# Kernel optimization log

Measured on AMD Instinct MI355X. Metric: run time of the kernel, lower is better.

The kernel has to match this reference:

```python
import jax, jax.numpy as jnp
import numpy as np

NF = 128  # latent_dim / number of filters


def setup_inputs() -> dict:
    key = jax.random.key(0)
    k1, k2, k3, k4 = jax.random.split(key, 4)
    B, H, W, C = 4, 64, 64, 128
    x = jax.random.normal(k1, (B, H, W, C), dtype=jnp.float32)
    y = jax.random.normal(k2, (B, H, W, C), dtype=jnp.float32)
    # 1x1 conv kernels (C_in, C_out) + biases, glorot-ish scale
    scale = 1.0 / np.sqrt(C)
    W1 = jax.random.normal(k3, (C, NF), dtype=jnp.float32) * scale
    W2 = jax.random.normal(k4, (C, NF), dtype=jnp.float32) * scale
    b1 = jnp.zeros((NF,), dtype=jnp.float32)
    b2 = jnp.zeros((NF,), dtype=jnp.float32)
    return {"x": x, "y": y, "W1": W1, "b1": b1, "W2": W2, "b2": b2}


def reference(x, y, W1, b1, W2, b2):
    B, H, Wd, C = x.shape
    hw = H * Wd
    # 1x1 convs == per-pixel matmul
    xq = jnp.einsum('bhwc,cf->bhwf', x, W1) + b1   # conv1(x)
    yk = jnp.einsum('bhwc,cf->bhwf', y, W2) + b2   # conv2(y)
    xq_r = xq.reshape(B, hw, NF)
    yk_r = yk.reshape(B, hw, NF)
    # A_ij = sigmoid(y_i . x_j), full (hw x hw) sigmoid attention
    A = jax.nn.sigmoid(jnp.einsum('bic,bjc->bij', yk_r, xq_r))
    out = jnp.einsum('bij,bjc->bic', A, yk_r).reshape(B, H, Wd, NF)
    # residual add of the *projected* x (matches original: x was overwritten by conv1)
    out = out + xq
    return out
```

## Files before the change

### kernel.cpp

```cpp
#include <hip/hip_runtime.h>
#include <hip/hip_bf16.h>
#include <stdint.h>

typedef float f32x16 __attribute__((ext_vector_type(16)));
typedef float f32x4  __attribute__((ext_vector_type(4)));
typedef short s16x8  __attribute__((ext_vector_type(8)));
typedef unsigned int u32x4 __attribute__((ext_vector_type(4)));

#define HWSZ   4096
#define NBATCH 4
#define LOG2E  1.44269504088896340736f

__device__ __forceinline__ unsigned short f2bf(float f) {
    unsigned u = __builtin_bit_cast(unsigned, f);
    u += 0x7FFFu + ((u >> 16) & 1u);
    return (unsigned short)(u >> 16);
}
__device__ __forceinline__ unsigned cvt_pk_bf16(float lo, float hi) {
    __hip_bfloat162 h = __float22bfloat162_rn(make_float2(lo, hi));
    return *reinterpret_cast<unsigned*>(&h);
}
__device__ __forceinline__ float sigm2(float s) {
    return __builtin_amdgcn_rcpf(1.f + __builtin_amdgcn_exp2f(-s));
}
__device__ __forceinline__ float bf_lo(unsigned u) {
    return __builtin_bit_cast(float, u << 16);
}
__device__ __forceinline__ float bf_hi(unsigned u) {
    return __builtin_bit_cast(float, u & 0xFFFF0000u);
}
__device__ __forceinline__ float bf2f(unsigned short u) {
    return __builtin_bit_cast(float, (unsigned)u << 16);
}

template<bool WF32>
__global__ __launch_bounds__(256, 2) void proj_kernel(
    const float* __restrict__ x, const float* __restrict__ y,
    const float* __restrict__ W1, const float* __restrict__ b1,
    const float* __restrict__ W2, const float* __restrict__ b2,
    float* __restrict__ xq_f32,
    unsigned short* __restrict__ xqu_bf,
    unsigned short* __restrict__ xq_bf,
    unsigned short* __restrict__ yk_bf,
    unsigned short* __restrict__ ykT_bf)
{
    __shared__ unsigned short Xlds[32][136];
    __shared__ unsigned short Ylds[32][136];
    __shared__ unsigned short Tlds[128][40];

    const int t    = threadIdx.x;
    const int lane = t & 63;
    const int w    = t >> 6;
    const int l31  = lane & 31;
    const int g    = lane >> 5;
    const int r0   = blockIdx.x * 32;
    const int b    = r0 >> 12;
    const int j0   = r0 & (HWSZ - 1);

    #pragma unroll
    for (int i = 0; i < 4; ++i) {
        int li = t + 256 * i;
        int row = li >> 5, c = (li & 31) * 4;
        float4 vx = *(const float4*)(x + (size_t)(r0 + row) * 128 + c);
        float4 vy = *(const float4*)(y + (size_t)(r0 + row) * 128 + c);
        *(uint2*)&Xlds[row][c] = make_uint2(cvt_pk_bf16(vx.x, vx.y), cvt_pk_bf16(vx.z, vx.w));
        *(uint2*)&Ylds[row][c] = make_uint2(cvt_pk_bf16(vy.x, vy.y), cvt_pk_bf16(vy.z, vy.w));
    }
    __syncthreads();

    const int m  = w >> 1;
    const int fh = w & 1;
    const float* Wm = m ? W2 : W1;
    const float* bm = m ? b2 : b1;
    const unsigned short* A0 = m ? &Ylds[0][0] : &Xlds[0][0];

    f32x16 acc[2];
    #pragma unroll
    for (int i = 0; i < 16; ++i) { acc[0][i] = 0.f; acc[1][i] = 0.f; }

    #pragma unroll
    for (int ks = 0; ks < 8; ++ks) {
        s16x8 bfr[2];
        #pragma unroll
        for (int ft = 0; ft < 2; ++ft) {
            const float* wp = Wm + (size_t)(ks * 16 + g * 8) * 128 + fh * 64 + ft * 32 + l31;
            #pragma unroll
            for (int i = 0; i < 8; ++i)
                bfr[ft][i] = (short)f2bf(wp[(size_t)i * 128]);
        }
        s16x8 af = *(const s16x8*)(A0 + (size_t)l31 * 136 + ks * 16 + g * 8);
        acc[0] = __builtin_amdgcn_mfma_f32_32x32x16_bf16(af, bfr[0], acc[0], 0, 0, 0);
        acc[1] = __builtin_amdgcn_mfma_f32_32x32x16_bf16(af, bfr[1], acc[1], 0, 0, 0);
    }

    const float bias_v[2] = { bm[fh * 64 + l31], bm[fh * 64 + 32 + l31] };

    if (m == 0) {
        #pragma unroll
        for (int ft = 0; ft < 2; ++ft) {
            int f = fh * 64 + ft * 32 + l31;
            #pragma unroll
            for (int r = 0; r < 16; ++r) {
                int row = (r & 3) + 8 * (r >> 2) + 4 * g;
                float v = acc[ft][r] + bias_v[ft];
                size_t o = (size_t)(r0 + row) * 128 + f;
                if (WF32) xq_f32[o] = v;
                else      xqu_bf[o] = f2bf(v);
                xq_bf[o] = f2bf(v * LOG2E);
            }
        }
    } else {
        #pragma unroll
        for (int ft = 0; ft < 2; ++ft) {
            int f = fh * 64 + ft * 32 + l31;
            #pragma unroll
            for (int rg = 0; rg < 4; ++rg) {
                float p0 = acc[ft][4 * rg + 0] + bias_v[ft];
                float p1 = acc[ft][4 * rg + 1] + bias_v[ft];
                float p2 = acc[ft][4 * rg + 2] + bias_v[ft];
                float p3 = acc[ft][4 * rg + 3] + bias_v[ft];
                int jb = 8 * rg + 4 * g;
                *(uint2*)&Tlds[f][jb] = make_uint2(cvt_pk_bf16(p0, p1), cvt_pk_bf16(p2, p3));
                size_t o = (size_t)(r0 + jb) * 128 + f;
                yk_bf[o]       = f2bf(p0);
                yk_bf[o + 128] = f2bf(p1);
                yk_bf[o + 256] = f2bf(p2);
                yk_bf[o + 384] = f2bf(p3);
            }
        }
    }
    __syncthreads();

    {
        int f  = t >> 1;
        int jh = (t & 1) * 16;
        unsigned short* dst = ykT_bf + ((size_t)(b * 128 + f)) * HWSZ + j0 + jh;
        #pragma unroll
        for (int c = 0; c < 2; ++c)
            *(s16x8*)(dst + c * 8) = *(const s16x8*)&Tlds[f][jh + c * 8];
    }
}

#define KT_STR   136
#define VT_STR   72
#define KT_BYTES (64 * KT_STR * 2)
#define VT_BYTES (128 * VT_STR * 2)
#define BUF_BYTES (KT_BYTES + VT_BYTES)

__global__ __launch_bounds__(256, 2) void attn128_kernel(
    const unsigned short* __restrict__ Kbf,
    const unsigned short* __restrict__ Qbf,
    const unsigned short* __restrict__ Vtbf,
    unsigned* __restrict__ outp)
{
    __shared__ __align__(16) char smem[2 * BUF_BYTES];

    const int t    = threadIdx.x;
    const int lane = t & 63;
    const int qt   = t >> 6;
    const int l31  = lane & 31;
    const int g    = lane >> 5;

    const int split  = blockIdx.x >> 7;
    const int r      = blockIdx.x & 127;
    const int b      = r >> 5;
    const int qb     = (r & 31) * 128;
    const int jBegin = split * (HWSZ / 4);
    const int nt     = (HWSZ / 4) / 64;

    s16x8 qfrag[8];
    {
        const unsigned short* qp =
            Qbf + (((size_t)(b * HWSZ + qb + 32 * qt + l31)) << 7) + g * 8;
        #pragma unroll
        for (int fs = 0; fs < 8; ++fs)
            qfrag[fs] = *(const s16x8*)(qp + fs * 16);
    }

    f32x16 acc[4];
    #pragma unroll
    for (int ft = 0; ft < 4; ++ft)
        #pragma unroll
        for (int i = 0; i < 16; ++i) acc[ft][i] = 0.f;

    f32x16 zv;
    #pragma unroll
    for (int i = 0; i < 16; ++i) zv[i] = 0.f;

    const unsigned short* Kbase = Kbf  + (((size_t)b * HWSZ) << 7);
    const unsigned short* Vbase = Vtbf + (((size_t)b) << 7) * HWSZ;

    const unsigned short* kSrc = Kbase + (size_t)(jBegin + (t >> 4)) * 128 + (t & 15) * 8;
    const unsigned short* vSrc = Vbase + (size_t)(t >> 3) * HWSZ + jBegin + (t & 7) * 8;
    const int kDst = (t >> 4) * KT_STR + (t & 15) * 8;
    const int vDst = (t >> 3) * VT_STR + (t & 7) * 8;

    {
        unsigned short* Kl = (unsigned short*)smem;
        unsigned short* Vl = (unsigned short*)(smem + KT_BYTES);
        #pragma unroll
        for (int i = 0; i < 4; ++i)
            *(s16x8*)(Kl + kDst + i * 16 * KT_STR) = *(const s16x8*)(kSrc + (size_t)i * 2048);
        #pragma unroll
        for (int i = 0; i < 4; ++i)
            *(s16x8*)(Vl + vDst + i * 32 * VT_STR) = *(const s16x8*)(vSrc + (size_t)i * 32 * HWSZ);
    }
    __syncthreads();

    int c = 0;
    for (int it = 0; it < nt; ++it) {
        const bool pre = (it + 1 < nt);
        const unsigned short* Kl = (const unsigned short*)(smem + c * BUF_BYTES);
        const unsigned short* Vl = (const unsigned short*)(smem + c * BUF_BYTES + KT_BYTES);

        s16x8 kf0[8], kf1[8];
        {
            const unsigned short* Krow = Kl + (size_t)l31 * KT_STR + g * 8;
            #pragma unroll
            for (int fs = 0; fs < 8; ++fs)
                kf0[fs] = *(const s16x8*)(Krow + fs * 16);
        }
        f32x16 s0a, s0b;
        __builtin_amdgcn_s_setprio(1);
        #pragma unroll
        for (int fs = 0; fs < 4; ++fs) {
            s0a = __builtin_amdgcn_mfma_f32_32x32x16_bf16(kf0[fs],     qfrag[fs],
                      fs == 0 ? zv : s0a, 0, 0, 0);
            s0b = __builtin_amdgcn_mfma_f32_32x32x16_bf16(kf0[fs + 4], qfrag[fs + 4],
                      fs == 0 ? zv : s0b, 0, 0, 0);
        }
        __builtin_amdgcn_s_setprio(0);

        {
            const unsigned short* Krow = Kl + (size_t)(32 + l31) * KT_STR + g * 8;
            #pragma unroll
            for (int fs = 0; fs < 8; ++fs)
                kf1[fs] = *(const s16x8*)(Krow + fs * 16);
        }
        s16x8 kr[4], vr[4];
        if (pre) {
            kSrc += 64 * 128;
            vSrc += 64;
            #pragma unroll
            for (int i = 0; i < 4; ++i)
                kr[i] = *(const s16x8*)(kSrc + (size_t)i * 2048);
            #pragma unroll
            for (int i = 0; i < 4; ++i)
                vr[i] = *(const s16x8*)(vSrc + (size_t)i * 32 * HWSZ);
        }

        f32x16 s1a, s1b;
        unsigned W0[2][4], W1[2][4];
        #pragma unroll
        for (int fs = 0; fs < 4; ++fs) {
            s1a = __builtin_amdgcn_mfma_f32_32x32x16_bf16(kf1[fs],     qfrag[fs],
                      fs == 0 ? zv : s1a, 0, 0, 0);
            s1b = __builtin_amdgcn_mfma_f32_32x32x16_bf16(kf1[fs + 4], qfrag[fs + 4],
                      fs == 0 ? zv : s1b, 0, 0, 0);
            const int rg = fs;
            float p0 = sigm2(s0a[4 * rg + 0] + s0b[4 * rg + 0]);
            float p1 = sigm2(s0a[4 * rg + 1] + s0b[4 * rg + 1]);
            float p2 = sigm2(s0a[4 * rg + 2] + s0b[4 * rg + 2]);
            float p3 = sigm2(s0a[4 * rg + 3] + s0b[4 * rg + 3]);
            W0[0][rg] = cvt_pk_bf16(p0, p1);
            W1[0][rg] = cvt_pk_bf16(p2, p3);
        }

        __builtin_amdgcn_s_setprio(1);
        #pragma unroll
        for (int s2 = 0; s2 < 2; ++s2) {
            unsigned a0 = W0[0][2 * s2], b0 = W0[0][2 * s2 + 1];
            unsigned a1 = W1[0][2 * s2], b1 = W1[0][2 * s2 + 1];
            asm("v_permlane32_swap_b32 %0, %1" : "+v"(a0), "+v"(b0));
            asm("v_permlane32_swap_b32 %0, %1" : "+v"(a1), "+v"(b1));
            u32x4 pw;
            pw[0] = a0; pw[1] = a1; pw[2] = b0; pw[3] = b1;
            s16x8 pf = __builtin_bit_cast(s16x8, pw);
            #pragma unroll
            for (int ft = 0; ft < 4; ++ft) {
                s16x8 vf = *(const s16x8*)(Vl + (size_t)(32 * ft + l31) * VT_STR + s2 * 16 + g * 8);
                acc[ft] = __builtin_amdgcn_mfma_f32_32x32x16_bf16(pf, vf, acc[ft], 0, 0, 0);
            }
            #pragma unroll
            for (int h = 0; h < 2; ++h) {
                const int rg = 2 * s2 + h;
                float p0 = sigm2(s1a[4 * rg + 0] + s1b[4 * rg + 0]);
                float p1 = sigm2(s1a[4 * rg + 1] + s1b[4 * rg + 1]);
                float p2 = sigm2(s1a[4 * rg + 2] + s1b[4 * rg + 2]);
                float p3 = sigm2(s1a[4 * rg + 3] + s1b[4 * rg + 3]);
                W0[1][rg] = cvt_pk_bf16(p0, p1);
                W1[1][rg] = cvt_pk_bf16(p2, p3);
            }
        }

        #pragma unroll
        for (int s2 = 0; s2 < 2; ++s2) {
            unsigned a0 = W0[1][2 * s2], b0 = W0[1][2 * s2 + 1];
            unsigned a1 = W1[1][2 * s2], b1 = W1[1][2 * s2 + 1];
            asm("v_permlane32_swap_b32 %0, %1" : "+v"(a0), "+v"(b0));
            asm("v_permlane32_swap_b32 %0, %1" : "+v"(a1), "+v"(b1));
            u32x4 pw;
            pw[0] = a0; pw[1] = a1; pw[2] = b0; pw[3] = b1;
            s16x8 pf = __builtin_bit_cast(s16x8, pw);
            const int ks = 2 + s2;
            #pragma unroll
            for (int ft = 0; ft < 4; ++ft) {
                s16x8 vf = *(const s16x8*)(Vl + (size_t)(32 * ft + l31) * VT_STR + ks * 16 + g * 8);
                acc[ft] = __builtin_amdgcn_mfma_f32_32x32x16_bf16(pf, vf, acc[ft], 0, 0, 0);
            }
        }
        __builtin_amdgcn_s_setprio(0);

        if (pre) {
            unsigned short* Kd = (unsigned short*)(smem + (c ^ 1) * BUF_BYTES);
            unsigned short* Vd = (unsigned short*)(smem + (c ^ 1) * BUF_BYTES + KT_BYTES);
            #pragma unroll
            for (int i = 0; i < 4; ++i)
                *(s16x8*)(Kd + kDst + i * 16 * KT_STR) = kr[i];
            #pragma unroll
            for (int i = 0; i < 4; ++i)
                *(s16x8*)(Vd + vDst + i * 32 * VT_STR) = vr[i];
        }
        __syncthreads();
        c ^= 1;
    }

    unsigned* op = outp + (size_t)split * ((size_t)NBATCH * HWSZ * 64);
    #pragma unroll
    for (int ft = 0; ft < 4; ++ft)
    #pragma unroll
    for (int pr = 0; pr < 8; ++pr) {
        int r2 = 2 * pr;
        int row = (r2 & 3) + 8 * (r2 >> 2) + 4 * g;
        int q = qb + 32 * qt + row;
        unsigned v = cvt_pk_bf16(acc[ft][r2], acc[ft][r2 + 1]);
        op[((size_t)(b * HWSZ + q) >> 1) * 128 + 32 * ft + l31] = v;
    }
}

template<bool SPLIT>
__global__ __launch_bounds__(256, 2) void attn_kernel(
    const unsigned short* __restrict__ Kbf,
    const unsigned short* __restrict__ Qbf,
    const unsigned short* __restrict__ Vtbf,
    const float* __restrict__ resid,
    float* __restrict__ outp)
{
    __shared__ __align__(16) char smem[2 * BUF_BYTES];

    const int t    = threadIdx.x;
    const int lane = t & 63;
    const int w    = t >> 6;
    const int qt   = w & 1;
    const int jt   = w >> 1;
    const int l31  = lane & 31;
    const int g    = lane >> 5;

    int bid = blockIdx.x;
    int half = 0;
    if (SPLIT) { half = bid >> 8; bid &= 255; }
    const int b      = bid >> 6;
    const int qb     = (bid & 63) * 64;
    const int jBegin = half * (HWSZ / 2);
    const int nt     = (SPLIT ? HWSZ / 2 : HWSZ) / 64;

    s16x8 qfrag[8];
    {
        const unsigned short* qp =
            Qbf + (((size_t)(b * HWSZ + qb + 32 * qt + l31)) << 7) + g * 8;
        #pragma unroll
        for (int fs = 0; fs < 8; ++fs)
            qfrag[fs] = *(const s16x8*)(qp + fs * 16);
    }

    f32x16 acc[4];
    #pragma unroll
    for (int ft = 0; ft < 4; ++ft)
        #pragma unroll
        for (int i = 0; i < 16; ++i) acc[ft][i] = 0.f;

    const unsigned short* Kbase = Kbf  + (((size_t)b * HWSZ) << 7);
    const unsigned short* Vbase = Vtbf + (((size_t)b) << 7) * HWSZ;

    const unsigned short* kSrc = Kbase + (size_t)(jBegin + (t >> 4)) * 128 + (t & 15) * 8;
    const unsigned short* vSrc = Vbase + (size_t)(t >> 3) * HWSZ + jBegin + (t & 7) * 8;
    const int kDst = (t >> 4) * KT_STR + (t & 15) * 8;
    const int vDst = (t >> 3) * VT_STR + (t & 7) * 8;

    {
        unsigned short* Kl = (unsigned short*)smem;
        unsigned short* Vl = (unsigned short*)(smem + KT_BYTES);
        #pragma unroll
        for (int i = 0; i < 4; ++i)
            *(s16x8*)(Kl + kDst + i * 16 * KT_STR) = *(const s16x8*)(kSrc + (size_t)i * 2048);
        #pragma unroll
        for (int i = 0; i < 4; ++i)
            *(s16x8*)(Vl + vDst + i * 32 * VT_STR) = *(const s16x8*)(vSrc + (size_t)i * 32 * HWSZ);
    }
    __syncthreads();

    int c = 0;
    for (int it = 0; it < nt; ++it) {
        const bool pre = (it + 1 < nt);
        s16x8 kr[4], vr[4];
        if (pre) {
            kSrc += 64 * 128;
            vSrc += 64;
            #pragma unroll
            for (int i = 0; i < 4; ++i)
                kr[i] = *(const s16x8*)(kSrc + (size_t)i * 2048);
            #pragma unroll
            for (int i = 0; i < 4; ++i)
                vr[i] = *(const s16x8*)(vSrc + (size_t)i * 32 * HWSZ);
        }

        const unsigned short* Kl = (const unsigned short*)(smem + c * BUF_BYTES);
        const unsigned short* Vl = (const unsigned short*)(smem + c * BUF_BYTES + KT_BYTES);

        f32x16 sa, sb;
        #pragma unroll
        for (int i = 0; i < 16; ++i) { sa[i] = 0.f; sb[i] = 0.f; }
        const unsigned short* Krow = Kl + (size_t)(32 * jt + l31) * KT_STR + g * 8;
        __builtin_amdgcn_s_setprio(1);
        #pragma unroll
        for (int fs = 0; fs < 4; ++fs) {
            sa = __builtin_amdgcn_mfma_f32_32x32x16_bf16(
                     *(const s16x8*)(Krow + fs * 16), qfrag[fs], sa, 0, 0, 0);
            sb = __builtin_amdgcn_mfma_f32_32x32x16_bf16(
                     *(const s16x8*)(Krow + (fs + 4) * 16), qfrag[fs + 4], sb, 0, 0, 0);
        }
        __builtin_amdgcn_s_setprio(0);

        unsigned W0[4], W1[4];
        #pragma unroll
        for (int rg = 0; rg < 4; ++rg) {
            float p0 = sigm2(sa[4 * rg + 0] + sb[4 * rg + 0]);
            float p1 = sigm2(sa[4 * rg + 1] + sb[4 * rg + 1]);
            float p2 = sigm2(sa[4 * rg + 2] + sb[4 * rg + 2]);
            float p3 = sigm2(sa[4 * rg + 3] + sb[4 * rg + 3]);
            W0[rg] = cvt_pk_bf16(p0, p1);
            W1[rg] = cvt_pk_bf16(p2, p3);
        }

        #pragma unroll
        for (int s2 = 0; s2 < 2; ++s2) {
            unsigned a0 = W0[2 * s2], b0 = W0[2 * s2 + 1];
            unsigned a1 = W1[2 * s2], b1 = W1[2 * s2 + 1];
            asm("v_permlane32_swap_b32 %0, %1" : "+v"(a0), "+v"(b0));
            asm("v_permlane32_swap_b32 %0, %1" : "+v"(a1), "+v"(b1));
            u32x4 pw;
            pw[0] = a0; pw[1] = a1; pw[2] = b0; pw[3] = b1;
            s16x8 pf = __builtin_bit_cast(s16x8, pw);
            const int ks = 2 * jt + s2;
            __builtin_amdgcn_s_setprio(1);
            #pragma unroll
            for (int ft = 0; ft < 4; ++ft) {
                s16x8 vf = *(const s16x8*)(Vl + (size_t)(32 * ft + l31) * VT_STR + ks * 16 + g * 8);
                acc[ft] = __builtin_amdgcn_mfma_f32_32x32x16_bf16(pf, vf, acc[ft], 0, 0, 0);
            }
            __builtin_amdgcn_s_setprio(0);
        }

        if (pre) {
            unsigned short* Kd = (unsigned short*)(smem + (c ^ 1) * BUF_BYTES);
            unsigned short* Vd = (unsigned short*)(smem + (c ^ 1) * BUF_BYTES + KT_BYTES);
            #pragma unroll
            for (int i = 0; i < 4; ++i)
                *(s16x8*)(Kd + kDst + i * 16 * KT_STR) = kr[i];
            #pragma unroll
            for (int i = 0; i < 4; ++i)
                *(s16x8*)(Vd + vDst + i * 32 * VT_STR) = vr[i];
        }
        __syncthreads();
        c ^= 1;
    }

    float* red = (float*)smem;
    if (jt == 1) {
        #pragma unroll
        for (int ft = 0; ft < 4; ++ft)
        #pragma unroll
        for (int r = 0; r < 16; ++r) {
            int row = (r & 3) + 8 * (r >> 2) + 4 * g;
            red[qt * 4096 + row * 128 + 32 * ft + l31] = acc[ft][r];
        }
    }
    __syncthreads();
    if (jt == 0) {
        float* op = outp + (SPLIT ? (size_t)half * ((size_t)NBATCH * HWSZ * 128) : 0);
        #pragma unroll
        for (int ft = 0; ft < 4; ++ft)
        #pragma unroll
        for (int r = 0; r < 16; ++r) {
            int row = (r & 3) + 8 * (r >> 2) + 4 * g;
            float v = acc[ft][r] + red[qt * 4096 + row * 128 + 32 * ft + l31];
            int q = qb + 32 * qt + row;
            size_t o = (((size_t)(b * HWSZ + q)) << 7) + 32 * ft + l31;
            if (SPLIT) op[o] = v;
            else       op[o] = v + resid[o];
        }
    }
}

__global__ __launch_bounds__(256, 1) void reduce2_kernel(
    const float* __restrict__ p0, const float* __restrict__ p1, float* outp)
{
    int i = blockIdx.x * 256 + threadIdx.x;
    f32x4 a = ((const f32x4*)p0)[i];
    f32x4 b = ((const f32x4*)p1)[i];
    f32x4 c = ((f32x4*)outp)[i];
    ((f32x4*)outp)[i] = a + b + c;
}

__global__ __launch_bounds__(256, 1) void reduce4bf_kernel(
    const unsigned* __restrict__ parts, const unsigned short* __restrict__ xqu,
    float* __restrict__ outp)
{
    const size_t NU = (size_t)NBATCH * HWSZ * 64;
    size_t j0 = ((size_t)blockIdx.x * 256 + threadIdx.x) * 4;
    f32x4 lo, hi;
    #pragma unroll
    for (int e = 0; e < 4; ++e) { lo[e] = 0.f; hi[e] = 0.f; }
    #pragma unroll
    for (int k = 0; k < 4; ++k) {
        u32x4 v = *(const u32x4*)(parts + k * NU + j0);
        #pragma unroll
        for (int e = 0; e < 4; ++e) {
            lo[e] += bf_lo(v[e]);
            hi[e] += bf_hi(v[e]);
        }
    }
    size_t p  = j0 >> 7;
    int    f0 = (int)(j0 & 127);
    size_t o0 = (p * 2) * 128 + f0;
    const ushort4 r0 = *(const ushort4*)(xqu + o0);
    const ushort4 r1 = *(const ushort4*)(xqu + o0 + 128);
    lo[0] += bf2f(r0.x); lo[1] += bf2f(r0.y); lo[2] += bf2f(r0.z); lo[3] += bf2f(r0.w);
    hi[0] += bf2f(r1.x); hi[1] += bf2f(r1.y); hi[2] += bf2f(r1.z); hi[3] += bf2f(r1.w);
    *(f32x4*)(outp + o0)       = lo;
    *(f32x4*)(outp + o0 + 128) = hi;
}

extern "C" void kernel_launch(void* const* d_in, const int* in_sizes, int n_in,
                              void* d_out, int out_size, void* d_ws, size_t ws_size,
                              hipStream_t stream) {
    const float* x  = (const float*)d_in[0];
    const float* y  = (const float*)d_in[1];
    const float* W1 = (const float*)d_in[2];
    const float* b1 = (const float*)d_in[3];
    const float* W2 = (const float*)d_in[4];
    const float* b2 = (const float*)d_in[5];
    float* out = (float*)d_out;

    const size_t NELEM = (size_t)NBATCH * HWSZ * 128;
    unsigned short* xq_bf  = (unsigned short*)d_ws;
    unsigned short* yk_bf  = xq_bf + NELEM;
    unsigned short* ykT_bf = yk_bf + NELEM;
    unsigned short* xqu_bf = ykT_bf + NELEM;
    unsigned* partu = (unsigned*)(xqu_bf + NELEM);
    float* part = (float*)(ykT_bf + NELEM);

    if (ws_size >= NELEM * 16) {
        proj_kernel<false><<<(int)(NBATCH * HWSZ / 32), 256, 0, stream>>>(
            x, y, W1, b1, W2, b2, nullptr, xqu_bf, xq_bf, yk_bf, ykT_bf);
        attn128_kernel<<<512, 256, 0, stream>>>(xq_bf, yk_bf, ykT_bf, partu);
        reduce4bf_kernel<<<(int)(NELEM / 2048), 256, 0, stream>>>(partu, xqu_bf, out);
    } else if (ws_size >= NELEM * 14) {
        proj_kernel<true><<<(int)(NBATCH * HWSZ / 32), 256, 0, stream>>>(
            x, y, W1, b1, W2, b2, out, nullptr, xq_bf, yk_bf, ykT_bf);
        attn_kernel<true><<<512, 256, 0, stream>>>(xq_bf, yk_bf, ykT_bf, out, part);
        reduce2_kernel<<<(int)(NELEM / 1024), 256, 0, stream>>>(part, part + NELEM, out);
    } else {
        proj_kernel<true><<<(int)(NBATCH * HWSZ / 32), 256, 0, stream>>>(
            x, y, W1, b1, W2, b2, out, nullptr, xq_bf, yk_bf, ykT_bf);
        attn_kernel<false><<<256, 256, 0, stream>>>(xq_bf, yk_bf, ykT_bf, out, out);
    }
}
```

Measured before the change: 60.83 us.

## Fuse split-K reduction into attention kernel via last-block atomic counter

The attention kernel now does the 4-way split reduction itself. Each block bumps a per-query-tile atomic counter, and the last of the four splits to finish sums the bf16 partials, adds the projected residual and writes the fp32 output. This removes the separate reduce4bf launch and its pass over global memory. In exchange it adds a threadfence and atomics, counters that proj_kernel resets, serialized reduce work in the last-arriving blocks, and a larger workspace requirement. The fallback fp32 attention paths are removed.

```diff
diff --git a/kernel.cpp b/kernel.cpp
--- a/kernel.cpp
+++ b/kernel.cpp
@@ -33,16 +33,15 @@
     return __builtin_bit_cast(float, (unsigned)u << 16);
 }
 
-template<bool WF32>
 __global__ __launch_bounds__(256, 2) void proj_kernel(
     const float* __restrict__ x, const float* __restrict__ y,
     const float* __restrict__ W1, const float* __restrict__ b1,
     const float* __restrict__ W2, const float* __restrict__ b2,
-    float* __restrict__ xq_f32,
     unsigned short* __restrict__ xqu_bf,
     unsigned short* __restrict__ xq_bf,
     unsigned short* __restrict__ yk_bf,
-    unsigned short* __restrict__ ykT_bf)
+    unsigned short* __restrict__ ykT_bf,
+    unsigned* __restrict__ cnt)
 {
     __shared__ unsigned short Xlds[32][136];
     __shared__ unsigned short Ylds[32][136];
@@ -57,6 +56,8 @@
     const int b    = r0 >> 12;
     const int j0   = r0 & (HWSZ - 1);
 
+    if (blockIdx.x == 0 && t < 128) cnt[t] = 0;
+
     #pragma unroll
     for (int i = 0; i < 4; ++i) {
         int li = t + 256 * i;
@@ -104,9 +105,8 @@
                 int row = (r & 3) + 8 * (r >> 2) + 4 * g;
                 float v = acc[ft][r] + bias_v[ft];
                 size_t o = (size_t)(r0 + row) * 128 + f;
-                if (WF32) xq_f32[o] = v;
-                else      xqu_bf[o] = f2bf(v);
-                xq_bf[o] = f2bf(v * LOG2E);
+                xqu_bf[o] = f2bf(v);
+                xq_bf[o]  = f2bf(v * LOG2E);
             }
         }
     } else {
@@ -147,11 +147,15 @@
 #define VT_BYTES (128 * VT_STR * 2)
 #define BUF_BYTES (KT_BYTES + VT_BYTES)
 
+template<bool FUSED>
 __global__ __launch_bounds__(256, 2) void attn128_kernel(
     const unsigned short* __restrict__ Kbf,
     const unsigned short* __restrict__ Qbf,
     const unsigned short* __restrict__ Vtbf,
-    unsigned* __restrict__ outp)
+    unsigned* __restrict__ outp,
+    const unsigned short* __restrict__ xqu,
+    float* __restrict__ outf,
+    unsigned* __restrict__ cnt)
 {
     __shared__ __align__(16) char smem[2 * BUF_BYTES];
 
@@ -325,7 +329,8 @@
         c ^= 1;
     }
 
-    unsigned* op = outp + (size_t)split * ((size_t)NBATCH * HWSZ * 64);
+    const size_t NU = (size_t)NBATCH * HWSZ * 64;
+    unsigned* op = outp + (size_t)split * NU;
     #pragma unroll
     for (int ft = 0; ft < 4; ++ft)
     #pragma unroll
@@ -336,180 +341,43 @@
         unsigned v = cvt_pk_bf16(acc[ft][r2], acc[ft][r2 + 1]);
         op[((size_t)(b * HWSZ + q) >> 1) * 128 + 32 * ft + l31] = v;
     }
-}
-
-template<bool SPLIT>
-__global__ __launch_bounds__(256, 2) void attn_kernel(
-    const unsigned short* __restrict__ Kbf,
-    const unsigned short* __restrict__ Qbf,
-    const unsigned short* __restrict__ Vtbf,
-    const float* __restrict__ resid,
-    float* __restrict__ outp)
-{
-    __shared__ __align__(16) char smem[2 * BUF_BYTES];
-
-    const int t    = threadIdx.x;
-    const int lane = t & 63;
-    const int w    = t >> 6;
-    const int qt   = w & 1;
-    const int jt   = w >> 1;
-    const int l31  = lane & 31;
-    const int g    = lane >> 5;
-
-    int bid = blockIdx.x;
-    int half = 0;
-    if (SPLIT) { half = bid >> 8; bid &= 255; }
-    const int b      = bid >> 6;
-    const int qb     = (bid & 63) * 64;
-    const int jBegin = half * (HWSZ / 2);
-    const int nt     = (SPLIT ? HWSZ / 2 : HWSZ) / 64;
-
-    s16x8 qfrag[8];
-    {
-        const unsigned short* qp =
-            Qbf + (((size_t)(b * HWSZ + qb + 32 * qt + l31)) << 7) + g * 8;
-        #pragma unroll
-        for (int fs = 0; fs < 8; ++fs)
-            qfrag[fs] = *(const s16x8*)(qp + fs * 16);
-    }
-
-    f32x16 acc[4];
-    #pragma unroll
-    for (int ft = 0; ft < 4; ++ft)
-        #pragma unroll
-        for (int i = 0; i < 16; ++i) acc[ft][i] = 0.f;
-
-    const unsigned short* Kbase = Kbf  + (((size_t)b * HWSZ) << 7);
-    const unsigned short* Vbase = Vtbf + (((size_t)b) << 7) * HWSZ;
-
-    const unsigned short* kSrc = Kbase + (size_t)(jBegin + (t >> 4)) * 128 + (t & 15) * 8;
-    const unsigned short* vSrc = Vbase + (size_t)(t >> 3) * HWSZ + jBegin + (t & 7) * 8;
-    const int kDst = (t >> 4) * KT_STR + (t & 15) * 8;
-    const int vDst = (t >> 3) * VT_STR + (t & 7) * 8;
-
-    {
-        unsigned short* Kl = (unsigned short*)smem;
-        unsigned short* Vl = (unsigned short*)(smem + KT_BYTES);
-        #pragma unroll
-        for (int i = 0; i < 4; ++i)
-            *(s16x8*)(Kl + kDst + i * 16 * KT_STR) = *(const s16x8*)(kSrc + (size_t)i * 2048);
-        #pragma unroll
-        for (int i = 0; i < 4; ++i)
-            *(s16x8*)(Vl + vDst + i * 32 * VT_STR) = *(const s16x8*)(vSrc + (size_t)i * 32 * HWSZ);
-    }
-    __syncthreads();
-
-    int c = 0;
-    for (int it = 0; it < nt; ++it) {
-        const bool pre = (it + 1 < nt);
-        s16x8 kr[4], vr[4];
-        if (pre) {
-            kSrc += 64 * 128;
-            vSrc += 64;
-            #pragma unroll
-            for (int i = 0; i < 4; ++i)
-                kr[i] = *(const s16x8*)(kSrc + (size_t)i * 2048);
-            #pragma unroll
-            for (int i = 0; i < 4; ++i)
-                vr[i] = *(const s16x8*)(vSrc + (size_t)i * 32 * HWSZ);
-        }
-
-        const unsigned short* Kl = (const unsigned short*)(smem + c * BUF_BYTES);
-        const unsigned short* Vl = (const unsigned short*)(smem + c * BUF_BYTES + KT_BYTES);
-
-        f32x16 sa, sb;
-        #pragma unroll
-        for (int i = 0; i < 16; ++i) { sa[i] = 0.f; sb[i] = 0.f; }
-        const unsigned short* Krow = Kl + (size_t)(32 * jt + l31) * KT_STR + g * 8;
-        __builtin_amdgcn_s_setprio(1);
-        #pragma unroll
-        for (int fs = 0; fs < 4; ++fs) {
-            sa = __builtin_amdgcn_mfma_f32_32x32x16_bf16(
-                     *(const s16x8*)(Krow + fs * 16), qfrag[fs], sa, 0, 0, 0);
-            sb = __builtin_amdgcn_mfma_f32_32x32x16_bf16(
-                     *(const s16x8*)(Krow + (fs + 4) * 16), qfrag[fs + 4], sb, 0, 0, 0);
-        }
-        __builtin_amdgcn_s_setprio(0);
-
-        unsigned W0[4], W1[4];
-        #pragma unroll
-        for (int rg = 0; rg < 4; ++rg) {
-            float p0 = sigm2(sa[4 * rg + 0] + sb[4 * rg + 0]);
-            float p1 = sigm2(sa[4 * rg + 1] + sb[4 * rg + 1]);
-            float p2 = sigm2(sa[4 * rg + 2] + sb[4 * rg + 2]);
-            float p3 = sigm2(sa[4 * rg + 3] + sb[4 * rg + 3]);
-            W0[rg] = cvt_pk_bf16(p0, p1);
-            W1[rg] = cvt_pk_bf16(p2, p3);
-        }
-
-        #pragma unroll
-        for (int s2 = 0; s2 < 2; ++s2) {
-            unsigned a0 = W0[2 * s2], b0 = W0[2 * s2 + 1];
-            unsigned a1 = W1[2 * s2], b1 = W1[2 * s2 + 1];
-            asm("v_permlane32_swap_b32 %0, %1" : "+v"(a0), "+v"(b0));
-            asm("v_permlane32_swap_b32 %0, %1" : "+v"(a1), "+v"(b1));
-            u32x4 pw;
-            pw[0] = a0; pw[1] = a1; pw[2] = b0; pw[3] = b1;
-            s16x8 pf = __builtin_bit_cast(s16x8, pw);
-            const int ks = 2 * jt + s2;
-            __builtin_amdgcn_s_setprio(1);
-            #pragma unroll
-            for (int ft = 0; ft < 4; ++ft) {
-                s16x8 vf = *(const s16x8*)(Vl + (size_t)(32 * ft + l31) * VT_STR + ks * 16 + g * 8);
-                acc[ft] = __builtin_amdgcn_mfma_f32_32x32x16_bf16(pf, vf, acc[ft], 0, 0, 0);
-            }
-            __builtin_amdgcn_s_setprio(0);
-        }
-
-        if (pre) {
-            unsigned short* Kd = (unsigned short*)(smem + (c ^ 1) * BUF_BYTES);
-            unsigned short* Vd = (unsigned short*)(smem + (c ^ 1) * BUF_BYTES + KT_BYTES);
-            #pragma unroll
-            for (int i = 0; i < 4; ++i)
-                *(s16x8*)(Kd + kDst + i * 16 * KT_STR) = kr[i];
-            #pragma unroll
-            for (int i = 0; i < 4; ++i)
-                *(s16x8*)(Vd + vDst + i * 32 * VT_STR) = vr[i];
-        }
+
+    if (FUSED) {
+        __threadfence();
+        __shared__ unsigned lastv;
+        if (t == 0) lastv = atomicAdd(&cnt[r], 1u);
         __syncthreads();
-        c ^= 1;
-    }
-
-    float* red = (float*)smem;
-    if (jt == 1) {
-        #pragma unroll
-        for (int ft = 0; ft < 4; ++ft)
-        #pragma unroll
-        for (int r = 0; r < 16; ++r) {
-            int row = (r & 3) + 8 * (r >> 2) + 4 * g;
-            red[qt * 4096 + row * 128 + 32 * ft + l31] = acc[ft][r];
-        }
-    }
-    __syncthreads();
-    if (jt == 0) {
-        float* op = outp + (SPLIT ? (size_t)half * ((size_t)NBATCH * HWSZ * 128) : 0);
-        #pragma unroll
-        for (int ft = 0; ft < 4; ++ft)
-        #pragma unroll
-        for (int r = 0; r < 16; ++r) {
-            int row = (r & 3) + 8 * (r >> 2) + 4 * g;
-            float v = acc[ft][r] + red[qt * 4096 + row * 128 + 32 * ft + l31];
-            int q = qb + 32 * qt + row;
-            size_t o = (((size_t)(b * HWSZ + q)) << 7) + 32 * ft + l31;
-            if (SPLIT) op[o] = v;
-            else       op[o] = v + resid[o];
-        }
-    }
-}
-
-__global__ __launch_bounds__(256, 1) void reduce2_kernel(
-    const float* __restrict__ p0, const float* __restrict__ p1, float* outp)
-{
-    int i = blockIdx.x * 256 + threadIdx.x;
-    f32x4 a = ((const f32x4*)p0)[i];
-    f32x4 b = ((const f32x4*)p1)[i];
-    f32x4 c = ((f32x4*)outp)[i];
-    ((f32x4*)outp)[i] = a + b + c;
+        if (lastv == 3u) {
+            const size_t gbase = ((size_t)(b * HWSZ + qb) >> 1) * 128;
+            #pragma unroll
+            for (int ch = 0; ch < 8; ++ch) {
+                int idx = ch * 1024 + t * 4;
+                f32x4 lo, hi;
+                #pragma unroll
+                for (int e = 0; e < 4; ++e) { lo[e] = 0.f; hi[e] = 0.f; }
+                #pragma unroll
+                for (int k = 0; k < 4; ++k) {
+                    const unsigned* pp = outp + (size_t)k * NU + gbase + idx;
+                    #pragma unroll
+                    for (int e = 0; e < 4; ++e) {
+                        unsigned v = __hip_atomic_load(pp + e, __ATOMIC_RELAXED,
+                                                       __HIP_MEMORY_SCOPE_AGENT);
+                        lo[e] += bf_lo(v);
+                        hi[e] += bf_hi(v);
+                    }
+                }
+                size_t p  = (gbase + idx) >> 7;
+                int    f0 = idx & 127;
+                size_t o0 = (p * 2) * 128 + f0;
+                const ushort4 ra = *(const ushort4*)(xqu + o0);
+                const ushort4 rb = *(const ushort4*)(xqu + o0 + 128);
+                lo[0] += bf2f(ra.x); lo[1] += bf2f(ra.y); lo[2] += bf2f(ra.z); lo[3] += bf2f(ra.w);
+                hi[0] += bf2f(rb.x); hi[1] += bf2f(rb.y); hi[2] += bf2f(rb.z); hi[3] += bf2f(rb.w);
+                *(f32x4*)(outf + o0)       = lo;
+                *(f32x4*)(outf + o0 + 128) = hi;
+            }
+        }
+    }
 }
 
 __global__ __launch_bounds__(256, 1) void reduce4bf_kernel(
@@ -558,21 +426,17 @@
     unsigned short* ykT_bf = yk_bf + NELEM;
     unsigned short* xqu_bf = ykT_bf + NELEM;
     unsigned* partu = (unsigned*)(xqu_bf + NELEM);
-    float* part = (float*)(ykT_bf + NELEM);
-
-    if (ws_size >= NELEM * 16) {
-        proj_kernel<false><<<(int)(NBATCH * HWSZ / 32), 256, 0, stream>>>(
-            x, y, W1, b1, W2, b2, nullptr, xqu_bf, xq_bf, yk_bf, ykT_bf);
-        attn128_kernel<<<512, 256, 0, stream>>>(xq_bf, yk_bf, ykT_bf, partu);
+    unsigned* cnt   = partu + 4 * (NELEM / 2);
+
+    proj_kernel<<<(int)(NBATCH * HWSZ / 32), 256, 0, stream>>>(
+        x, y, W1, b1, W2, b2, xqu_bf, xq_bf, yk_bf, ykT_bf, cnt);
+
+    if (ws_size >= NELEM * 16 + 4096) {
+        attn128_kernel<true><<<512, 256, 0, stream>>>(
+            xq_bf, yk_bf, ykT_bf, partu, xqu_bf, out, cnt);
+    } else {
+        attn128_kernel<false><<<512, 256, 0, stream>>>(
+            xq_bf, yk_bf, ykT_bf, partu, xqu_bf, out, cnt);
         reduce4bf_kernel<<<(int)(NELEM / 2048), 256, 0, stream>>>(partu, xqu_bf, out);
-    } else if (ws_size >= NELEM * 14) {
-        proj_kernel<true><<<(int)(NBATCH * HWSZ / 32), 256, 0, stream>>>(
-            x, y, W1, b1, W2, b2, out, nullptr, xq_bf, yk_bf, ykT_bf);
-        attn_kernel<true><<<512, 256, 0, stream>>>(xq_bf, yk_bf, ykT_bf, out, part);
-        reduce2_kernel<<<(int)(NELEM / 1024), 256, 0, stream>>>(part, part + NELEM, out);
-    } else {
-        proj_kernel<true><<<(int)(NBATCH * HWSZ / 32), 256, 0, stream>>>(
-            x, y, W1, b1, W2, b2, out, nullptr, xq_bf, yk_bf, ykT_bf);
-        attn_kernel<false><<<256, 256, 0, stream>>>(xq_bf, yk_bf, ykT_bf, out, out);
-    }
-}
+    }
+}
```

Result: slower. 115.9 us (+90.6%).
